# Kernel tuning notes

Measured on AMD Instinct MI355X. Metric: run time of the kernel, lower is better.

The kernel has to match this reference:

```python
import jax, jax.numpy as jnp
import numpy as np

L_IN, L_FREQ, L_OUT = 128, 64, 64
C_IN, C_OUT, T_DIM = 64, 64, 256
SPIN = 1

# ---------- self-contained spin-weighted SHT (MW sampling), replacing s2fft ----------

def _mw_thetas(L, extended):
    n = 2 * L - 1 if extended else L
    return (2 * np.arange(n) + 1) * np.pi / (2 * L - 1)

def _wigner_d_stack(L, thetas, n):
    # d^l_{m,n}(theta) = <l,m| exp(-i theta Jy) |l,n>, computed via eigh of the
    # Hermitian angular-momentum operator Jy. Output (ntheta, L, 2L-1), m at col L-1+m.
    nth = len(thetas)
    out = np.zeros((nth, L, 2 * L - 1), dtype=np.float64)
    for l in range(abs(n), L):
        dim = 2 * l + 1
        m = np.arange(-l, l).astype(np.float64)
        ap = np.sqrt(l * (l + 1.0) - m * (m + 1.0))
        Jy = np.zeros((dim, dim), dtype=np.complex128)
        i = np.arange(dim - 1)
        Jy[i + 1, i] = -0.5j * ap
        Jy[i, i + 1] = 0.5j * ap
        lam, V = np.linalg.eigh(Jy)
        coeff = V * np.conj(V[l + n, :])[None, :]
        phases = np.exp(-1j * np.outer(lam, thetas))
        out[:, l, L - 1 - l:L + l] = (coeff @ phases).T.real
    return out

def _mw_quad_weights(L):
    # per-theta weights on the mirror-extended grid: q_t = (1/(2L-1)) sum_k w(k) e^{ik theta_t}
    # with w(k) = int_0^pi e^{ik t} sin(t) dt
    k = np.arange(-(L - 1), L)
    den = np.where(np.abs(k) == 1, 1, 1 - k * k).astype(np.float64)
    w = np.where(k % 2 == 0, 2.0 / den, 0.0).astype(np.complex128)
    w[k == 1] = 0.5j * np.pi
    w[k == -1] = -0.5j * np.pi
    th = _mw_thetas(L, True)
    return ((w[None, :] * np.exp(1j * np.outer(th, k))).sum(1) / (2 * L - 1)).real

# transform kernels are constants (built once at import, numpy)
_D_FWD = jnp.asarray(_wigner_d_stack(L_IN, _mw_thetas(L_IN, True), -SPIN) * _mw_quad_weights(L_IN)[:, None, None], jnp.float32)
_D_INV = jnp.asarray(_wigner_d_stack(L_OUT, _mw_thetas(L_OUT, False), -SPIN), jnp.float32)
_CL_IN = jnp.asarray(((-1.0) ** SPIN) * np.sqrt((2 * np.arange(L_IN) + 1) / (4 * np.pi)), jnp.float32)
_CL_OUT = jnp.asarray(((-1.0) ** SPIN) * np.sqrt((2 * np.arange(L_OUT) + 1) / (4 * np.pi)), jnp.float32)
_m_all = np.arange(-(L_IN - 1), L_IN)
_PARITY = jnp.asarray(np.where((_m_all + SPIN) % 2 == 0, 1.0, -1.0), jnp.float32)

def sht_forward(x):
    # x: (L_IN, 2*L_IN-1, C) real spatial -> flm: (L_IN, 2*L_IN-1, C) complex, m at L_IN-1+m
    nphi = 2 * L_IN - 1
    ftm = jnp.fft.fftshift(jnp.fft.fft(x, axis=1), axes=1) * (2 * jnp.pi / nphi)
    # mirror extension in theta with (-1)^(m+spin) parity (all channels at once)
    g_ext = jnp.concatenate([ftm, _PARITY[None, :, None] * ftm[::-1][1:]], axis=0)
    flm = jnp.einsum('tlm,tmc->lmc', _D_FWD, g_ext)
    return flm * _CL_IN[:, None, None]

def sht_inverse(flm):
    # flm: (L_OUT, 2*L_OUT-1, C) complex -> (L_OUT, 2*L_OUT-1, C) real spatial
    ftm = jnp.einsum('tlm,lmc->tmc', _D_INV, flm * _CL_OUT[:, None, None])
    return (jnp.fft.ifft(jnp.fft.ifftshift(ftm, axes=1), axis=1) * (2 * L_OUT - 1)).real

def resize_flm(flm, l_in, l_out):
    # centered truncation / zero-pad of (L, 2L-1, C) harmonic coefficients
    if l_out <= l_in:
        d = l_in - l_out
        return flm[:l_out, d:d + 2 * l_out - 1]
    d = l_out - l_in
    return jnp.pad(flm, ((0, d), (d, d), (0, 0)))

# ---------- inputs and parameters ----------

def setup_inputs():
    key = jax.random.key(0)
    ks = jax.random.split(key, 12)
    n = lambda i, shape, s: jax.random.normal(ks[i], shape, jnp.float32) * s
    return {
        'x': jax.random.normal(ks[0], (L_IN, 2 * L_IN - 1, C_IN), jnp.float32),
        't_emb': jax.random.normal(ks[1], (T_DIM,), jnp.float32),
        'spec_conv_w': n(2, (C_IN, C_OUT), (1.0 / C_IN) ** 0.5),
        'spec_conv_b': jnp.zeros((C_OUT,), jnp.float32),
        'spec_wr': n(3, (L_FREQ, C_IN, C_OUT), (0.5 / C_IN) ** 0.5),
        'spec_wi': n(4, (L_FREQ, C_IN, C_OUT), (0.5 / C_IN) ** 0.5),
        'spec_tr_w': n(5, (T_DIM, L_FREQ), (1.0 / T_DIM) ** 0.5),
        'spec_tr_b': jnp.zeros((L_FREQ,), jnp.float32),
        'spec_ti_w': n(6, (T_DIM, L_FREQ), (1.0 / T_DIM) ** 0.5),
        'spec_ti_b': jnp.zeros((L_FREQ,), jnp.float32),
        'spat_conv1_w': n(7, (C_IN, C_OUT), (1.0 / C_IN) ** 0.5),
        'spat_conv1_b': jnp.zeros((C_OUT,), jnp.float32),
        'spat_t_w': n(8, (T_DIM, 2 * C_OUT), (1.0 / T_DIM) ** 0.5),
        'spat_t_b': jnp.zeros((2 * C_OUT,), jnp.float32),
        'spat_weight': n(9, (C_OUT, C_OUT), 0.01),
        'spat_conv2_w': n(10, (C_OUT, C_OUT), (1.0 / C_OUT) ** 0.5),
        'spat_conv2_b': jnp.zeros((C_OUT,), jnp.float32),
        'ln_scale': jnp.ones((C_OUT,), jnp.float32),
        'ln_bias': jnp.zeros((C_OUT,), jnp.float32),
    }

def reference(x, t_emb, spec_conv_w, spec_conv_b, spec_wr, spec_wi, spec_tr_w, spec_tr_b, spec_ti_w, spec_ti_b, spat_conv1_w, spat_conv1_b, spat_t_w, spat_t_b, spat_weight, spat_conv2_w, spat_conv2_b, ln_scale, ln_bias):
    # ----- SphericalSpectralTimeConv branch -----
    flm = sht_forward(x)                                   # (L_IN, 2L_IN-1, C_IN) complex
    flm = resize_flm(flm, L_IN, L_FREQ)                    # (L_FREQ, 2L_FREQ-1, C_IN)
    conv_flm = jnp.einsum('lmi,io->lmo', flm, spec_conv_w) + spec_conv_b
    t_c = (t_emb @ spec_tr_w + spec_tr_b) + 1j * (t_emb @ spec_ti_w + spec_ti_b)   # (L_FREQ,)
    w = t_c[:, None, None] * (spec_wr + 1j * spec_wi)      # (L_FREQ, C_IN, C_OUT)
    flm = jnp.einsum('lmi,lio->lmo', flm, w) + conv_flm
    xs = sht_inverse(resize_flm(flm, L_FREQ, L_OUT))       # (L_OUT, 2L_OUT-1, C_OUT) real
    xs = xs / (jnp.linalg.norm(xs, axis=-1, keepdims=True) + 1e-6)
    # ----- SpatialTimeConv branch (path='down') -----
    h = jnp.einsum('lmi,io->lmo', x, spat_conv1_w) + spat_conv1_b
    t = t_emb @ spat_t_w + spat_t_b
    w_t, b_t = t[:C_OUT], t[C_OUT:]
    h = jnp.einsum('lmi,io->lmo', h, w_t[None, :] * spat_weight)
    h = sht_inverse(resize_flm(sht_forward(h), L_IN, L_OUT))
    h = jnp.einsum('lmi,io->lmo', h, spat_conv2_w) + spat_conv2_b + b_t
    # ----- combine: add, gelu, LayerNorm (eps=1e-6 over channels) -----
    y = jax.nn.gelu(xs + h)
    mu = jnp.mean(y, axis=-1, keepdims=True)
    var = jnp.var(y, axis=-1, keepdims=True)
    return (y - mu) * jax.lax.rsqrt(var + 1e-6) * ln_scale + ln_bias
```

## Files before the change

### kernel.cpp

```cpp
#include <hip/hip_runtime.h>
#include <math.h>

#define DPI 3.141592653589793238462643383279502884

__device__ __forceinline__ float wave_sum64(float v) {
#pragma unroll
  for (int off = 32; off > 0; off >>= 1) v += __shfl_xor(v, off, 64);
  return v;
}

__device__ __forceinline__ float gelu_tanh(float v) {
  float u = 0.7978845608028654f * (v + 0.044715f * v * v * v);
  return 0.5f * v * (1.0f + tanhf(u));
}

#define CN255F ((float)(-2.0 * DPI / 255.0))
#define CN127F ((float)(2.0 * DPI / 127.0))


__device__ __forceinline__ void dft_block(int idx, int tid, const float* __restrict__ x,
                                          float* __restrict__ Are, float* __restrict__ Aim,
                                          float* __restrict__ Bre, float* __restrict__ Bim,
                                          char* sm) {
  float* xs_ = (float*)sm;
  int t = idx >> 2, ph = (idx >> 1) & 1, mh = idx & 1;
  float* ore = ph ? Bre : Are;
  float* oim = ph ? Bim : Aim;
  int pbase = ph * 128;
  int Ktot = ph ? 127 : 128;
  int cg_ = tid & 15, mg = tid >> 4;
  float wr[2], wi[2], rc[2], rs[2];
#pragma unroll
  for (int j = 0; j < 2; ++j) {
    int m = mh * 32 + mg * 2 + j;
    __sincosf(CN255F * (float)m, &rs[j], &rc[j]);
    int r0 = (m * pbase) % 255;
    __sincosf(CN255F * (float)r0, &wi[j], &wr[j]);
  }
  float accr[2][4], acci[2][4];
#pragma unroll
  for (int j = 0; j < 2; ++j)
#pragma unroll
    for (int q = 0; q < 4; ++q) { accr[j][q] = 0.f; acci[j][q] = 0.f; }
  for (int k0 = 0; k0 < Ktot; k0 += 64) {
    int kn = (Ktot - k0 < 64) ? Ktot - k0 : 64;
    __syncthreads();
    {
      const float4* src = (const float4*)(x + ((size_t)t * 255 + pbase + k0) * 64);
      float4* dst = (float4*)xs_;
      int lim = kn * 16;
#pragma unroll
      for (int q = 0; q < 4; ++q) {
        int fidx = tid + q * 256;
        if (fidx < lim) dst[fidx] = src[fidx];
      }
    }
    __syncthreads();
#pragma unroll 2
    for (int k = 0; k < kn; ++k) {
      float4 xv = *(const float4*)&xs_[k * 64 + cg_ * 4];
      float xv4[4] = {xv.x, xv.y, xv.z, xv.w};
#pragma unroll
      for (int j = 0; j < 2; ++j) {
#pragma unroll
        for (int q = 0; q < 4; ++q) {
          accr[j][q] = fmaf(xv4[q], wr[j], accr[j][q]);
          acci[j][q] = fmaf(xv4[q], wi[j], acci[j][q]);
        }
        float nw = wr[j] * rc[j] - wi[j] * rs[j];
        wi[j] = fmaf(wr[j], rs[j], wi[j] * rc[j]);
        wr[j] = nw;
      }
    }
  }
#pragma unroll
  for (int j = 0; j < 2; ++j) {
    int mi = mh * 32 + mg * 2 + j;
    size_t ob = ((size_t)t * 64 + mi) * 64 + cg_ * 4;
    *(float4*)(ore + ob) = make_float4(accr[j][0], accr[j][1], accr[j][2], accr[j][3]);
    *(float4*)(oim + ob) = make_float4(acci[j][0], acci[j][1], acci[j][2], acci[j][3]);
  }
}

__device__ __forceinline__ void wigner_block(int wb, int tid, float* __restrict__ Deff,
                                             float* __restrict__ Dinv, char* sm) {
  float* LF = (float*)sm;
  double* red = (double*)(sm + 512);
  float* clf = (float*)(sm + 1024);
  int mode = (wb < 128) ? 0 : 1;
  int t, mm;
  if (mode == 0) { t = wb; mm = tid; }
  else { mm = wb - 128; t = (tid < 64) ? tid : 63; }
  if (tid < 64) clf[tid] = (float)(-sqrt((2.0 * tid + 1.0) / (4.0 * DPI)));
  if (tid < 128) LF[tid] = (tid == 0) ? 0.f : logf((float)tid);
  __syncthreads();
  for (int s = 1; s < 128; s <<= 1) {
    float add = (tid < 128 && tid >= s) ? LF[tid - s] : 0.f;
    __syncthreads();
    if (tid < 128) LF[tid] += add;
    __syncthreads();
  }
  double denomN = (mode == 0) ? 255.0 : 127.0;
  double beta = (2.0 * t + 1.0) * DPI / denomN;
  float coeff = 1.0f;
  if (mode == 0) {
    if (tid < 63) {
      int k = 2 * (tid + 1);
      red[tid] = 8.0 * cos((double)k * beta) / (1.0 - (double)k * (double)k);
    } else if (tid == 63) {
      red[63] = 4.0;
    }
    __syncthreads();
    for (int s = 32; s > 0; s >>= 1) {
      if (tid < s) red[tid] += red[tid + s];
      __syncthreads();
    }
    double s = red[0] / 255.0;
    if (t == 127) s *= 0.5;
    coeff = (float)(s * (2.0 * DPI / 255.0));
  }
  bool active = (mode == 0) ? (tid < 127) : (tid < 64);
  if (!active) return;
  int m = mm - 63;
  double chd, shd;
  sincos(0.5 * beta, &shd, &chd);
  float cbf = (float)cos(beta);
  float chf = (float)chd, shf = (float)shd;
  int am = (m < 0) ? -m : m;
  int l0v = (am > 1) ? am : 1;
  float seed;
  if (m == 0) {
    seed = -1.4142135623730951f * shf * chf;
  } else {
    int j = am;
    float lch = logf(chf), lsh = logf(shf);
    float e0 = 0.5f * (LF[2 * j] - LF[j - 1] - LF[j + 1]);
    float expo = (m >= 1) ? e0 + (float)(j - 1) * lch + (float)(j + 1) * lsh
                          : e0 + (float)(j + 1) * lch + (float)(j - 1) * lsh;
    float sv = __expf(expo);
    seed = (m >= 1 && ((m + 1) & 1)) ? -sv : sv;
  }
  float dl = seed, dm1 = 0.0f, S_cur = 0.0f;
  float mf = (float)m;
  for (int l = 0; l < 64; ++l) {
    float val = 0.0f;
    if (l >= l0v) {
      val = dl * coeff * clf[l];
      float Ld = (float)l, lp = Ld + 1.0f;
      float S_next = sqrtf((lp * lp - mf * mf) * (lp * lp - 1.0f));
      float num1 = (2.0f * Ld + 1.0f) * (Ld * lp * cbf + mf);
      float dn = (num1 * dl - lp * S_cur * dm1) / (Ld * S_next);
      dm1 = dl; dl = dn; S_cur = S_next;
    }
    if (mode == 0) Deff[((size_t)t * 127 + mm) * 64 + l] = val;
    else Dinv[((size_t)mm * 64 + l) * 64 + t] = val;
  }
}

__device__ __forceinline__ void a2_block(int l, int tid, const float* __restrict__ temb,
                                         const float* __restrict__ trw, const float* __restrict__ trb,
                                         const float* __restrict__ tiw, const float* __restrict__ tib,
                                         const float* __restrict__ scw, const float* __restrict__ swr,
                                         const float* __restrict__ swi, float2* __restrict__ A2,
                                         char* sm) {
  float* fb1 = (float*)sm;
  float* fb2 = (float*)(sm + 1024);
  fb1[tid] = temb[tid] * trw[tid * 64 + l];
  fb2[tid] = temb[tid] * tiw[tid * 64 + l];
  __syncthreads();
  for (int s = 128; s > 0; s >>= 1) {
    if (tid < s) { fb1[tid] += fb1[tid + s]; fb2[tid] += fb2[tid + s]; }
    __syncthreads();
  }
  float tr = fb1[0] + trb[l], ti = fb2[0] + tib[l];
  int o = tid & 63, iq = tid >> 6;
  for (int i = iq * 16; i < iq * 16 + 16; ++i) {
    int idx = (l * 64 + i) * 64 + o;
    float r = swr[idx], s2 = swi[idx];
    A2[idx] = make_float2(scw[i * 64 + o] + tr * r - ti * s2, tr * s2 + ti * r);
  }
}

__device__ __forceinline__ void m_block(int j, int tid, const float* __restrict__ temb,
                                        const float* __restrict__ stw, const float* __restrict__ stb,
                                        const float* __restrict__ c1w, const float* __restrict__ c1b,
                                        const float* __restrict__ sweight, float* __restrict__ Mm,
                                        float* __restrict__ bias2, char* sm) {
  float* fb1 = (float*)sm;
  float* fb2 = (float*)(sm + 1024);
  int o = tid & 63, part = tid >> 6;
  float p = 0.f;
  for (int k = part * 64; k < part * 64 + 64; ++k)
    p = fmaf(temb[k], stw[k * 128 + o], p);
  fb1[part * 64 + o] = p;
  __syncthreads();
  if (part == 0) fb2[o] = fb1[o] + fb1[64 + o] + fb1[128 + o] + fb1[192 + o] + stb[o];
  __syncthreads();
  float tvo = fb2[o];
  float q = 0.f;
  for (int i = part * 16; i < part * 16 + 16; ++i)
    q = fmaf(c1w[j * 64 + i], sweight[i * 64 + o], q);
  __syncthreads();
  fb1[part * 64 + o] = q;
  __syncthreads();
  if (part == 0) Mm[j * 64 + o] = tvo * (fb1[o] + fb1[64 + o] + fb1[128 + o] + fb1[192 + o]);
  if (j == 0) {
    float bq = 0.f;
    for (int i = part * 16; i < part * 16 + 16; ++i)
      bq = fmaf(c1b[i], sweight[i * 64 + o], bq);
    __syncthreads();
    fb1[part * 64 + o] = bq;
    __syncthreads();
    if (part == 0) bias2[o] = tvo * (fb1[o] + fb1[64 + o] + fb1[128 + o] + fb1[192 + o]);
  }
}

__device__ __forceinline__ void tv_block(int tid, const float* __restrict__ temb,
                                         const float* __restrict__ stw, const float* __restrict__ stb,
                                         float* __restrict__ tv, char* sm) {
  float* fb1 = (float*)sm;
  int o = tid & 127, part = tid >> 7;
  float p = 0.f;
  for (int k = part * 128; k < part * 128 + 128; ++k)
    p = fmaf(temb[k], stw[k * 128 + o], p);
  fb1[part * 128 + o] = p;
  __syncthreads();
  if (part == 0) tv[o] = fb1[o] + fb1[128 + o] + stb[o];
}

__global__ __launch_bounds__(256, 2) void ct_pre(
    const float* __restrict__ x, const float* __restrict__ temb,
    const float* __restrict__ trw, const float* __restrict__ trb,
    const float* __restrict__ tiw, const float* __restrict__ tib,
    const float* __restrict__ stw, const float* __restrict__ stb,
    const float* __restrict__ scw, const float* __restrict__ swr,
    const float* __restrict__ swi, const float* __restrict__ c1w,
    const float* __restrict__ c1b, const float* __restrict__ sweight,
    float* __restrict__ Deff, float* __restrict__ Dinv,
    float2* __restrict__ A2, float* __restrict__ Mm,
    float* __restrict__ bias2, float* __restrict__ tv,
    float* __restrict__ ftmA_re, float* __restrict__ ftmA_im,
    float* __restrict__ ftmB_re, float* __restrict__ ftmB_im) {
  __shared__ __align__(16) char sm[16384];
  int vb = blockIdx.x;
  int tid = threadIdx.x;
  if (vb < 255) wigner_block(vb, tid, Deff, Dinv, sm);
  else if (vb < 319) a2_block(vb - 255, tid, temb, trw, trb, tiw, tib, scw, swr, swi, A2, sm);
  else if (vb < 383) m_block(vb - 319, tid, temb, stw, stb, c1w, c1b, sweight, Mm, bias2, sm);
  else if (vb < 384) tv_block(tid, temb, stw, stb, tv, sm);
  else dft_block(vb - 384, tid, x, ftmA_re, ftmA_im, ftmB_re, ftmB_im, sm);
}

__global__ __launch_bounds__(256) void ct_projf(const float* __restrict__ Deff,
                                                const float* __restrict__ fAre,
                                                const float* __restrict__ fAim,
                                                const float* __restrict__ fBre,
                                                const float* __restrict__ fBim,
                                                float* __restrict__ flmA_re, float* __restrict__ flmA_im,
                                                float* __restrict__ flmB_re, float* __restrict__ flmB_im) {
  __shared__ float Dsh[64][32];
  __shared__ float fr_[64][64], fi_[64][64];
  int mm = blockIdx.x, lh = blockIdx.y, th = blockIdx.z;
  float* ore = th ? flmB_re : flmA_re;
  float* oim = th ? flmB_im : flmA_im;
  int tb = th * 64;
  int mi = (mm >= 63) ? (mm - 63) : (63 - mm);
  float csign = (mm >= 63) ? 1.0f : -1.0f;
  int tid = threadIdx.x;
  int cg_ = tid & 15, lg = tid >> 4;
  for (int e = tid; e < 64 * 32; e += 256) {
    int r = e >> 5, li = e & 31;
    Dsh[r][li] = Deff[((size_t)(tb + r) * 127 + mm) * 64 + lh * 32 + li];
  }
  for (int e = tid; e < 64 * 64; e += 256) {
    int r = e >> 6, c = e & 63;
    size_t idx = ((size_t)(tb + r) * 64 + mi) * 64 + c;
    fr_[r][c] = fAre[idx] + fBre[idx];
    fi_[r][c] = csign * (fAim[idx] + fBim[idx]);
  }
  __syncthreads();
  float ar[2][4], ai[2][4];
#pragma unroll
  for (int li = 0; li < 2; ++li)
#pragma unroll
    for (int q = 0; q < 4; ++q) { ar[li][q] = 0.f; ai[li][q] = 0.f; }
#pragma unroll 4
  for (int k = 0; k < 64; ++k) {
    float4 fr4 = *(const float4*)&fr_[k][cg_ * 4];
    float4 fi4 = *(const float4*)&fi_[k][cg_ * 4];
    float2 d2 = *(const float2*)&Dsh[k][lg * 2];
    float frv[4] = {fr4.x, fr4.y, fr4.z, fr4.w};
    float fiv[4] = {fi4.x, fi4.y, fi4.z, fi4.w};
    float dv[2] = {d2.x, d2.y};
#pragma unroll
    for (int li = 0; li < 2; ++li)
#pragma unroll
      for (int q = 0; q < 4; ++q) {
        ar[li][q] = fmaf(dv[li], frv[q], ar[li][q]);
        ai[li][q] = fmaf(dv[li], fiv[q], ai[li][q]);
      }
  }
#pragma unroll
  for (int li = 0; li < 2; ++li) {
    size_t row = ((size_t)mm * 64 + lh * 32 + lg * 2 + li) * 64 + cg_ * 4;
    *(float4*)(ore + row) = make_float4(ar[li][0], ar[li][1], ar[li][2], ar[li][3]);
    *(float4*)(oim + row) = make_float4(ai[li][0], ai[li][1], ai[li][2], ai[li][3]);
  }
}

__global__ __launch_bounds__(256) void ct_mix(const float* __restrict__ flmA_re,
                                              const float* __restrict__ flmA_im,
                                              const float* __restrict__ flmB_re,
                                              const float* __restrict__ flmB_im,
                                              const float2* __restrict__ A2,
                                              const float* __restrict__ Mm,
                                              const float* __restrict__ scb,
                                              const float* __restrict__ bias2,
                                              const float* __restrict__ Deff,
                                              float* __restrict__ s_re, float* __restrict__ s_im,
                                              float* __restrict__ h_re, float* __restrict__ h_im) {
  __shared__ float Ar_[64][32], Ai_[64][32], Msh[64][32];
  __shared__ float Br_[64][65], Bi_[64][65];
  __shared__ float rb[256];
  int l = blockIdx.x, mh = blockIdx.y, oh = blockIdx.z;
  int tid = threadIdx.x;
  int og = tid & 15, mg = tid >> 4;
  rb[tid] = (mh == 0 && tid < 128) ? Deff[((size_t)tid * 127 + 63) * 64 + l] : 0.f;
  __syncthreads();
  for (int s = 128; s > 0; s >>= 1) {
    if (tid < s) rb[tid] += rb[tid + s];
    __syncthreads();
  }
  float slv = rb[0];
  for (int e = tid; e < 64 * 32; e += 256) {
    int r = e >> 5, oi = e & 31;
    float2 aa = A2[((size_t)l * 64 + r) * 64 + oh * 32 + oi];
    Ar_[r][oi] = aa.x; Ai_[r][oi] = aa.y;
    Msh[r][oi] = Mm[r * 64 + oh * 32 + oi];
  }
  for (int e = tid; e < 64 * 64; e += 256) {
    int mi = e >> 6, i = e & 63;
    int gmm = mh * 64 + mi; if (gmm > 126) gmm = 126;
    size_t idx = ((size_t)gmm * 64 + l) * 64 + i;
    Br_[mi][i] = flmA_re[idx] + flmB_re[idx];
    Bi_[mi][i] = flmA_im[idx] + flmB_im[idx];
  }
  __syncthreads();
  int o0 = oh * 32 + og * 2;
  float b0[2] = {scb[o0], scb[o0 + 1]};
  float sr[4][2], si[4][2], hr[4][2], hi[4][2];
#pragma unroll
  for (int jm = 0; jm < 4; ++jm)
#pragma unroll
    for (int qo = 0; qo < 2; ++qo) {
      sr[jm][qo] = b0[qo]; si[jm][qo] = 0.f; hr[jm][qo] = 0.f; hi[jm][qo] = 0.f;
    }
#pragma unroll 4
  for (int k = 0; k < 64; ++k) {
    float2 ar2 = *(const float2*)&Ar_[k][og * 2];
    float2 ai2 = *(const float2*)&Ai_[k][og * 2];
    float2 mv2 = *(const float2*)&Msh[k][og * 2];
    float br4[4], bi4[4];
#pragma unroll
    for (int jm = 0; jm < 4; ++jm) {
      br4[jm] = Br_[mg * 4 + jm][k];
      bi4[jm] = Bi_[mg * 4 + jm][k];
    }
    float arv[2] = {ar2.x, ar2.y}, aiv[2] = {ai2.x, ai2.y}, mvv[2] = {mv2.x, mv2.y};
#pragma unroll
    for (int jm = 0; jm < 4; ++jm)
#pragma unroll
      for (int qo = 0; qo < 2; ++qo) {
        sr[jm][qo] = fmaf(br4[jm], arv[qo], sr[jm][qo]);
        sr[jm][qo] = fmaf(-bi4[jm], aiv[qo], sr[jm][qo]);
        si[jm][qo] = fmaf(br4[jm], aiv[qo], si[jm][qo]);
        si[jm][qo] = fmaf(bi4[jm], arv[qo], si[jm][qo]);
        hr[jm][qo] = fmaf(br4[jm], mvv[qo], hr[jm][qo]);
        hi[jm][qo] = fmaf(bi4[jm], mvv[qo], hi[jm][qo]);
      }
  }
  float bb[2] = {bias2[o0], bias2[o0 + 1]};
#pragma unroll
  for (int jm = 0; jm < 4; ++jm) {
    int gmm = mh * 64 + mg * 4 + jm;
    if (gmm > 126) continue;
    if (gmm == 63) {
#pragma unroll
      for (int qo = 0; qo < 2; ++qo)
        hr[jm][qo] = fmaf(255.0f * slv, bb[qo], hr[jm][qo]);
    }
    size_t row = ((size_t)gmm * 64 + l) * 64 + o0;
    *(float2*)(s_re + row) = make_float2(sr[jm][0], sr[jm][1]);
    *(float2*)(s_im + row) = make_float2(si[jm][0], si[jm][1]);
    *(float2*)(h_re + row) = make_float2(hr[jm][0], hr[jm][1]);
    *(float2*)(h_im + row) = make_float2(hi[jm][0], hi[jm][1]);
  }
}

__global__ __launch_bounds__(256) void ct_proji(const float* __restrict__ Dinv,
                                                const float* __restrict__ s_re,
                                                const float* __restrict__ s_im,
                                                const float* __restrict__ h_re,
                                                const float* __restrict__ h_im,
                                                float* __restrict__ fos_re, float* __restrict__ fos_im,
                                                float* __restrict__ foh_re, float* __restrict__ foh_im) {
  __shared__ float Dsh[64][64];
  __shared__ float Br_[64][32], Bi_[64][32];
  int mm = blockIdx.x, br = blockIdx.y, ch = blockIdx.z;
  const float* ire = br ? h_re : s_re;
  const float* iim = br ? h_im : s_im;
  float* ore = br ? foh_re : fos_re;
  float* oim = br ? foh_im : fos_im;
  int tid = threadIdx.x;
  int cg_ = tid & 15, tg = tid >> 4;
  for (int e = tid; e < 64 * 64; e += 256) {
    int r = e >> 6, tt = e & 63;
    Dsh[r][tt] = Dinv[((size_t)mm * 64 + r) * 64 + tt];
  }
  for (int e = tid; e < 64 * 32; e += 256) {
    int r = e >> 5, cc = e & 31;
    size_t idx = ((size_t)mm * 64 + r) * 64 + ch * 32 + cc;
    Br_[r][cc] = ire[idx];
    Bi_[r][cc] = iim[idx];
  }
  __syncthreads();
  float ar[4][2], ai[4][2];
#pragma unroll
  for (int j = 0; j < 4; ++j)
#pragma unroll
    for (int q = 0; q < 2; ++q) { ar[j][q] = 0.f; ai[j][q] = 0.f; }
#pragma unroll 4
  for (int k = 0; k < 64; ++k) {
    float4 d4 = *(const float4*)&Dsh[k][tg * 4];
    float2 fr2 = *(const float2*)&Br_[k][cg_ * 2];
    float2 fi2 = *(const float2*)&Bi_[k][cg_ * 2];
    float dv[4] = {d4.x, d4.y, d4.z, d4.w};
    float frv[2] = {fr2.x, fr2.y}, fiv[2] = {fi2.x, fi2.y};
#pragma unroll
    for (int j = 0; j < 4; ++j)
#pragma unroll
      for (int q = 0; q < 2; ++q) {
        ar[j][q] = fmaf(dv[j], frv[q], ar[j][q]);
        ai[j][q] = fmaf(dv[j], fiv[q], ai[j][q]);
      }
  }
#pragma unroll
  for (int j = 0; j < 4; ++j) {
    int t = tg * 4 + j;
    size_t ob = ((size_t)t * 127 + mm) * 64 + ch * 32 + cg_ * 2;
    *(float2*)(ore + ob) = make_float2(ar[j][0], ar[j][1]);
    *(float2*)(oim + ob) = make_float2(ai[j][0], ai[j][1]);
  }
}

__global__ __launch_bounds__(256) void ct_idft(const float* __restrict__ fos_re,
                                               const float* __restrict__ fos_im,
                                               const float* __restrict__ foh_re,
                                               const float* __restrict__ foh_im,
                                               float* __restrict__ xsbA, float* __restrict__ xsbB,
                                               float* __restrict__ hsbA, float* __restrict__ hsbB) {
  __shared__ float Br_[32][64], Bi_[32][64];
  int t = blockIdx.x, br = blockIdx.y;
  int z = blockIdx.z;
  int ph = z >> 1, kh = z & 1;
  const float* fre = br ? foh_re : fos_re;
  const float* fim = br ? foh_im : fos_im;
  float* outp = br ? (kh ? hsbB : hsbA) : (kh ? xsbB : xsbA);
  int kbase = kh * 64;
  int Ktot = kh ? 63 : 64;
  int tid = threadIdx.x;
  int cg_ = tid & 15, pg = tid >> 4;
  float wc[4], ws[4], rc[4], rs[4];
#pragma unroll
  for (int j = 0; j < 4; ++j) {
    int gp = ph * 64 + pg * 4 + j; if (gp > 126) gp = 126;
    __sincosf(CN127F * (float)gp, &rs[j], &rc[j]);
    int r0 = ((kbase - 63) * gp) % 127;
    __sincosf(CN127F * (float)r0, &ws[j], &wc[j]);
  }
  float acc[4][4];
#pragma unroll
  for (int j = 0; j < 4; ++j)
#pragma unroll
    for (int q = 0; q < 4; ++q) acc[j][q] = 0.f;
  for (int k0 = 0; k0 < Ktot; k0 += 32) {
    int kn = (Ktot - k0 < 32) ? Ktot - k0 : 32;
    __syncthreads();
    for (int e = tid; e < 32 * 64; e += 256) {
      int r = e >> 6, j = e & 63;
      if (r < kn) {
        size_t bidx = ((size_t)t * 127 + kbase + k0 + r) * 64 + j;
        Br_[r][j] = fre[bidx]; Bi_[r][j] = fim[bidx];
      }
    }
    __syncthreads();
#pragma unroll 2
    for (int k = 0; k < kn; ++k) {
      float4 b_r = *(const float4*)&Br_[k][cg_ * 4];
      float4 b_i = *(const float4*)&Bi_[k][cg_ * 4];
      float brv[4] = {b_r.x, b_r.y, b_r.z, b_r.w};
      float biv[4] = {b_i.x, b_i.y, b_i.z, b_i.w};
#pragma unroll
      for (int j = 0; j < 4; ++j) {
#pragma unroll
        for (int q = 0; q < 4; ++q) {
          acc[j][q] = fmaf(brv[q], wc[j], acc[j][q]);
          acc[j][q] = fmaf(biv[q], -ws[j], acc[j][q]);
        }
        float nw = wc[j] * rc[j] - ws[j] * rs[j];
        ws[j] = fmaf(wc[j], rs[j], ws[j] * rc[j]);
        wc[j] = nw;
      }
    }
  }
#pragma unroll
  for (int j = 0; j < 4; ++j) {
    int gp = ph * 64 + pg * 4 + j;
    if (gp > 126) continue;
    *(float4*)(outp + ((size_t)t * 127 + gp) * 64 + cg_ * 4) =
        make_float4(acc[j][0], acc[j][1], acc[j][2], acc[j][3]);
  }
}

__global__ __launch_bounds__(256) void ct_fin(const float* __restrict__ xsbA,
                                              const float* __restrict__ xsbB,
                                              const float* __restrict__ hsbA,
                                              const float* __restrict__ hsbB,
                                              const float* __restrict__ c2w,
                                              const float* __restrict__ c2b,
                                              const float* __restrict__ tv,
                                              const float* __restrict__ lns,
                                              const float* __restrict__ lnb,
                                              float* __restrict__ out) {
  int w = threadIdx.x >> 6, lane = threadIdx.x & 63;
  size_t row = (size_t)blockIdx.x * 4 + w;
  size_t base = row * 64 + lane;
  float hv = hsbA[base] + hsbB[base];
  float xv = xsbA[base] + xsbB[base];
  float acc = c2b[lane] + tv[64 + lane];
#pragma unroll 16
  for (int i = 0; i < 64; ++i)
    acc = fmaf(__shfl(hv, i, 64), c2w[i * 64 + lane], acc);
  float ss = wave_sum64(xv * xv);
  xv = xv / (sqrtf(ss) + 1e-6f);
  float y = xv + acc;
  float g = gelu_tanh(y);
  float mu = wave_sum64(g) * (1.0f / 64.0f);
  float d = g - mu;
  float var = wave_sum64(d * d) * (1.0f / 64.0f);
  out[base] = d * rsqrtf(var + 1e-6f) * lns[lane] + lnb[lane];
}

extern "C" void kernel_launch(void* const* d_in, const int* in_sizes, int n_in,
                              void* d_out, int out_size, void* d_ws, size_t ws_size,
                              hipStream_t stream) {
  const float* x = (const float*)d_in[0];
  const float* temb = (const float*)d_in[1];
  const float* scw = (const float*)d_in[2];
  const float* scb = (const float*)d_in[3];
  const float* swr = (const float*)d_in[4];
  const float* swi = (const float*)d_in[5];
  const float* strw = (const float*)d_in[6];
  const float* strb = (const float*)d_in[7];
  const float* stiw = (const float*)d_in[8];
  const float* stib = (const float*)d_in[9];
  const float* c1w = (const float*)d_in[10];
  const float* c1b = (const float*)d_in[11];
  const float* stw = (const float*)d_in[12];
  const float* stb = (const float*)d_in[13];
  const float* sweight = (const float*)d_in[14];
  const float* c2w = (const float*)d_in[15];
  const float* c2b = (const float*)d_in[16];
  const float* lns = (const float*)d_in[17];
  const float* lnb = (const float*)d_in[18];
  float* out = (float*)d_out;

  char* base = (char*)d_ws;
  size_t off = 0;
  auto alloc = [&](size_t bytes) -> void* {
    void* p = base + off;
    off += (bytes + 255) & ~(size_t)255;
    return p;
  };
  float* tv = (float*)alloc(128 * sizeof(float));
  float* Mm = (float*)alloc(4096 * sizeof(float));
  float* bias2 = (float*)alloc(64 * sizeof(float));
  float2* A2 = (float2*)alloc(262144 * sizeof(float2));
  float* Deff = (float*)alloc(1040384 * sizeof(float));
  float* Dinv = (float*)alloc(520192 * sizeof(float));
  float* ftmA_re = (float*)alloc(524288 * sizeof(float));
  float* ftmA_im = (float*)alloc(524288 * sizeof(float));
  float* ftmB_re = (float*)alloc(524288 * sizeof(float));
  float* ftmB_im = (float*)alloc(524288 * sizeof(float));
  float* flmA_re = (float*)alloc(520192 * sizeof(float));
  float* flmA_im = (float*)alloc(520192 * sizeof(float));
  float* flmB_re = (float*)alloc(520192 * sizeof(float));
  float* flmB_im = (float*)alloc(520192 * sizeof(float));
  if (off > ws_size) return;
  float* s_re = ftmA_re;
  float* s_im = ftmA_im;
  float* h_re = ftmB_re;
  float* h_im = ftmB_im;
  float* fos_re = Deff;
  float* fos_im = Deff + 520192;
  float* foh_re = flmA_re;
  float* foh_im = flmA_im;
  float* xsbA = flmB_re;
  float* xsbB = flmB_im;
  float* hsbA = ftmA_re;
  float* hsbB = ftmA_im;

  hipLaunchKernelGGL(ct_pre, dim3(896), dim3(256), 0, stream,
                     x, temb, strw, strb, stiw, stib, stw, stb,
                     scw, swr, swi, c1w, c1b, sweight,
                     Deff, Dinv, A2, Mm, bias2, tv,
                     ftmA_re, ftmA_im, ftmB_re, ftmB_im);
  hipLaunchKernelGGL(ct_projf, dim3(127, 2, 2), dim3(256), 0, stream, Deff,
                     ftmA_re, ftmA_im, ftmB_re, ftmB_im,
                     flmA_re, flmA_im, flmB_re, flmB_im);
  hipLaunchKernelGGL(ct_mix, dim3(64, 2, 2), dim3(256), 0, stream,
                     flmA_re, flmA_im, flmB_re, flmB_im, A2, Mm, scb, bias2, Deff,
                     s_re, s_im, h_re, h_im);
  hipLaunchKernelGGL(ct_proji, dim3(127, 2, 2), dim3(256), 0, stream, Dinv,
                     s_re, s_im, h_re, h_im, fos_re, fos_im, foh_re, foh_im);
  hipLaunchKernelGGL(ct_idft, dim3(64, 2, 4), dim3(256), 0, stream,
                     fos_re, fos_im, foh_re, foh_im, xsbA, xsbB, hsbA, hsbB);
  hipLaunchKernelGGL(ct_fin, dim3(2032), dim3(256), 0, stream, xsbA, xsbB, hsbA, hsbB,
                     c2w, c2b, tv, lns, lnb, out);
}
```

Baseline: 193.9 us.

## Fuse six kernel launches into one persistent kernel with grid barriers

Merges the six pipeline stages (pre, forward projection, mixing, inverse projection, inverse DFT, final layernorm) into one persistent kernel. Blocks loop over per-stage tile indices and meet at atomic-counter grid barriers that are reset by a memset before launch. This removes inter-kernel launch gaps and tail drain. The cost is one large shared-memory allocation, which caps occupancy, plus spin-wait barriers that assume all blocks are co-resident. The Wigner recurrence also switches to fast reciprocal and sqrt intrinsics.

```diff
diff --git a/kernel.cpp b/kernel.cpp
--- a/kernel.cpp
+++ b/kernel.cpp
@@ -2,6 +2,8 @@
 #include <math.h>
 
 #define DPI 3.141592653589793238462643383279502884
+#define CN255F ((float)(-2.0 * DPI / 255.0))
+#define CN127F ((float)(2.0 * DPI / 127.0))
 
 __device__ __forceinline__ float wave_sum64(float v) {
 #pragma unroll
@@ -14,11 +16,21 @@
   return 0.5f * v * (1.0f + tanhf(u));
 }
 
-#define CN255F ((float)(-2.0 * DPI / 255.0))
-#define CN127F ((float)(2.0 * DPI / 127.0))
-
-
-__device__ __forceinline__ void dft_block(int idx, int tid, const float* __restrict__ x,
+__device__ __forceinline__ void gsync(unsigned* cnt, unsigned nb) {
+  __syncthreads();
+  if (threadIdx.x == 0) {
+    __threadfence();
+    atomicAdd(cnt, 1u);
+    while (__hip_atomic_load(cnt, __ATOMIC_RELAXED, __HIP_MEMORY_SCOPE_AGENT) < nb) {
+      __builtin_amdgcn_s_sleep(2);
+    }
+    __threadfence();
+  }
+  __syncthreads();
+}
+
+
+__device__ __forceinline__ void dft_phase(int idx, int tid, const float* __restrict__ x,
                                           float* __restrict__ Are, float* __restrict__ Aim,
                                           float* __restrict__ Bre, float* __restrict__ Bim,
                                           char* sm) {
@@ -82,7 +94,7 @@
   }
 }
 
-__device__ __forceinline__ void wigner_block(int wb, int tid, float* __restrict__ Deff,
+__device__ __forceinline__ void wigner_phase(int wb, int tid, float* __restrict__ Deff,
                                              float* __restrict__ Dinv, char* sm) {
   float* LF = (float*)sm;
   double* red = (double*)(sm + 512);
@@ -120,44 +132,45 @@
     coeff = (float)(s * (2.0 * DPI / 255.0));
   }
   bool active = (mode == 0) ? (tid < 127) : (tid < 64);
-  if (!active) return;
-  int m = mm - 63;
-  double chd, shd;
-  sincos(0.5 * beta, &shd, &chd);
-  float cbf = (float)cos(beta);
-  float chf = (float)chd, shf = (float)shd;
-  int am = (m < 0) ? -m : m;
-  int l0v = (am > 1) ? am : 1;
-  float seed;
-  if (m == 0) {
-    seed = -1.4142135623730951f * shf * chf;
-  } else {
-    int j = am;
-    float lch = logf(chf), lsh = logf(shf);
-    float e0 = 0.5f * (LF[2 * j] - LF[j - 1] - LF[j + 1]);
-    float expo = (m >= 1) ? e0 + (float)(j - 1) * lch + (float)(j + 1) * lsh
-                          : e0 + (float)(j + 1) * lch + (float)(j - 1) * lsh;
-    float sv = __expf(expo);
-    seed = (m >= 1 && ((m + 1) & 1)) ? -sv : sv;
-  }
-  float dl = seed, dm1 = 0.0f, S_cur = 0.0f;
-  float mf = (float)m;
-  for (int l = 0; l < 64; ++l) {
-    float val = 0.0f;
-    if (l >= l0v) {
-      val = dl * coeff * clf[l];
-      float Ld = (float)l, lp = Ld + 1.0f;
-      float S_next = sqrtf((lp * lp - mf * mf) * (lp * lp - 1.0f));
-      float num1 = (2.0f * Ld + 1.0f) * (Ld * lp * cbf + mf);
-      float dn = (num1 * dl - lp * S_cur * dm1) / (Ld * S_next);
-      dm1 = dl; dl = dn; S_cur = S_next;
-    }
-    if (mode == 0) Deff[((size_t)t * 127 + mm) * 64 + l] = val;
-    else Dinv[((size_t)mm * 64 + l) * 64 + t] = val;
-  }
-}
-
-__device__ __forceinline__ void a2_block(int l, int tid, const float* __restrict__ temb,
+  if (active) {
+    int m = mm - 63;
+    double chd, shd;
+    sincos(0.5 * beta, &shd, &chd);
+    float cbf = (float)cos(beta);
+    float chf = (float)chd, shf = (float)shd;
+    int am = (m < 0) ? -m : m;
+    int l0v = (am > 1) ? am : 1;
+    float seed;
+    if (m == 0) {
+      seed = -1.4142135623730951f * shf * chf;
+    } else {
+      int j = am;
+      float lch = logf(chf), lsh = logf(shf);
+      float e0 = 0.5f * (LF[2 * j] - LF[j - 1] - LF[j + 1]);
+      float expo = (m >= 1) ? e0 + (float)(j - 1) * lch + (float)(j + 1) * lsh
+                            : e0 + (float)(j + 1) * lch + (float)(j - 1) * lsh;
+      float sv = __expf(expo);
+      seed = (m >= 1 && ((m + 1) & 1)) ? -sv : sv;
+    }
+    float dl = seed, dm1 = 0.0f, S_cur = 0.0f;
+    float mf = (float)m;
+    for (int l = 0; l < 64; ++l) {
+      float val = 0.0f;
+      if (l >= l0v) {
+        val = dl * coeff * clf[l];
+        float Ld = (float)l, lp = Ld + 1.0f;
+        float S_next = __fsqrt_rn((lp * lp - mf * mf) * (lp * lp - 1.0f));
+        float num1 = (2.0f * Ld + 1.0f) * (Ld * lp * cbf + mf);
+        float dn = (num1 * dl - lp * S_cur * dm1) * __fdividef(1.0f, Ld * S_next);
+        dm1 = dl; dl = dn; S_cur = S_next;
+      }
+      if (mode == 0) Deff[((size_t)t * 127 + mm) * 64 + l] = val;
+      else Dinv[((size_t)mm * 64 + l) * 64 + t] = val;
+    }
+  }
+}
+
+__device__ __forceinline__ void a2_phase(int l, int tid, const float* __restrict__ temb,
                                          const float* __restrict__ trw, const float* __restrict__ trb,
                                          const float* __restrict__ tiw, const float* __restrict__ tib,
                                          const float* __restrict__ scw, const float* __restrict__ swr,
@@ -181,7 +194,7 @@
   }
 }
 
-__device__ __forceinline__ void m_block(int j, int tid, const float* __restrict__ temb,
+__device__ __forceinline__ void m_phase(int j, int tid, const float* __restrict__ temb,
                                         const float* __restrict__ stw, const float* __restrict__ stb,
                                         const float* __restrict__ c1w, const float* __restrict__ c1b,
                                         const float* __restrict__ sweight, float* __restrict__ Mm,
@@ -215,7 +228,7 @@
   }
 }
 
-__device__ __forceinline__ void tv_block(int tid, const float* __restrict__ temb,
+__device__ __forceinline__ void tv_phase(int tid, const float* __restrict__ temb,
                                          const float* __restrict__ stw, const float* __restrict__ stb,
                                          float* __restrict__ tv, char* sm) {
   float* fb1 = (float*)sm;
@@ -228,45 +241,21 @@
   if (part == 0) tv[o] = fb1[o] + fb1[128 + o] + stb[o];
 }
 
-__global__ __launch_bounds__(256, 2) void ct_pre(
-    const float* __restrict__ x, const float* __restrict__ temb,
-    const float* __restrict__ trw, const float* __restrict__ trb,
-    const float* __restrict__ tiw, const float* __restrict__ tib,
-    const float* __restrict__ stw, const float* __restrict__ stb,
-    const float* __restrict__ scw, const float* __restrict__ swr,
-    const float* __restrict__ swi, const float* __restrict__ c1w,
-    const float* __restrict__ c1b, const float* __restrict__ sweight,
-    float* __restrict__ Deff, float* __restrict__ Dinv,
-    float2* __restrict__ A2, float* __restrict__ Mm,
-    float* __restrict__ bias2, float* __restrict__ tv,
-    float* __restrict__ ftmA_re, float* __restrict__ ftmA_im,
-    float* __restrict__ ftmB_re, float* __restrict__ ftmB_im) {
-  __shared__ __align__(16) char sm[16384];
-  int vb = blockIdx.x;
-  int tid = threadIdx.x;
-  if (vb < 255) wigner_block(vb, tid, Deff, Dinv, sm);
-  else if (vb < 319) a2_block(vb - 255, tid, temb, trw, trb, tiw, tib, scw, swr, swi, A2, sm);
-  else if (vb < 383) m_block(vb - 319, tid, temb, stw, stb, c1w, c1b, sweight, Mm, bias2, sm);
-  else if (vb < 384) tv_block(tid, temb, stw, stb, tv, sm);
-  else dft_block(vb - 384, tid, x, ftmA_re, ftmA_im, ftmB_re, ftmB_im, sm);
-}
-
-__global__ __launch_bounds__(256) void ct_projf(const float* __restrict__ Deff,
-                                                const float* __restrict__ fAre,
-                                                const float* __restrict__ fAim,
-                                                const float* __restrict__ fBre,
-                                                const float* __restrict__ fBim,
-                                                float* __restrict__ flmA_re, float* __restrict__ flmA_im,
-                                                float* __restrict__ flmB_re, float* __restrict__ flmB_im) {
-  __shared__ float Dsh[64][32];
-  __shared__ float fr_[64][64], fi_[64][64];
-  int mm = blockIdx.x, lh = blockIdx.y, th = blockIdx.z;
+__device__ __forceinline__ void projf_phase(int mm, int lh, int th, int tid,
+                                            const float* __restrict__ Deff,
+                                            const float* __restrict__ fAre, const float* __restrict__ fAim,
+                                            const float* __restrict__ fBre, const float* __restrict__ fBim,
+                                            float* __restrict__ flmA_re, float* __restrict__ flmA_im,
+                                            float* __restrict__ flmB_re, float* __restrict__ flmB_im,
+                                            char* sm) {
+  float (*Dsh)[32] = (float(*)[32])(sm);
+  float (*fr_)[64] = (float(*)[64])(sm + 8192);
+  float (*fi_)[64] = (float(*)[64])(sm + 24576);
   float* ore = th ? flmB_re : flmA_re;
   float* oim = th ? flmB_im : flmA_im;
   int tb = th * 64;
   int mi = (mm >= 63) ? (mm - 63) : (63 - mm);
   float csign = (mm >= 63) ? 1.0f : -1.0f;
-  int tid = threadIdx.x;
   int cg_ = tid & 15, lg = tid >> 4;
   for (int e = tid; e < 64 * 32; e += 256) {
     int r = e >> 5, li = e & 31;
@@ -308,22 +297,21 @@
   }
 }
 
-__global__ __launch_bounds__(256) void ct_mix(const float* __restrict__ flmA_re,
-                                              const float* __restrict__ flmA_im,
-                                              const float* __restrict__ flmB_re,
-                                              const float* __restrict__ flmB_im,
-                                              const float2* __restrict__ A2,
-                                              const float* __restrict__ Mm,
-                                              const float* __restrict__ scb,
-                                              const float* __restrict__ bias2,
-                                              const float* __restrict__ Deff,
-                                              float* __restrict__ s_re, float* __restrict__ s_im,
-                                              float* __restrict__ h_re, float* __restrict__ h_im) {
-  __shared__ float Ar_[64][32], Ai_[64][32], Msh[64][32];
-  __shared__ float Br_[64][65], Bi_[64][65];
-  __shared__ float rb[256];
-  int l = blockIdx.x, mh = blockIdx.y, oh = blockIdx.z;
-  int tid = threadIdx.x;
+__device__ __forceinline__ void mix_phase(int l, int mh, int oh, int tid,
+                                          const float* __restrict__ flmA_re, const float* __restrict__ flmA_im,
+                                          const float* __restrict__ flmB_re, const float* __restrict__ flmB_im,
+                                          const float2* __restrict__ A2, const float* __restrict__ Mm,
+                                          const float* __restrict__ scb, const float* __restrict__ bias2,
+                                          const float* __restrict__ Deff,
+                                          float* __restrict__ s_re, float* __restrict__ s_im,
+                                          float* __restrict__ h_re, float* __restrict__ h_im,
+                                          char* sm) {
+  float (*Ar_)[32] = (float(*)[32])(sm);
+  float (*Ai_)[32] = (float(*)[32])(sm + 8192);
+  float (*Msh)[32] = (float(*)[32])(sm + 16384);
+  float (*Br_)[65] = (float(*)[65])(sm + 24576);
+  float (*Bi_)[65] = (float(*)[65])(sm + 41216);
+  float* rb = (float*)(sm + 57856);
   int og = tid & 15, mg = tid >> 4;
   rb[tid] = (mh == 0 && tid < 128) ? Deff[((size_t)tid * 127 + 63) * 64 + l] : 0.f;
   __syncthreads();
@@ -397,21 +385,20 @@
   }
 }
 
-__global__ __launch_bounds__(256) void ct_proji(const float* __restrict__ Dinv,
-                                                const float* __restrict__ s_re,
-                                                const float* __restrict__ s_im,
-                                                const float* __restrict__ h_re,
-                                                const float* __restrict__ h_im,
-                                                float* __restrict__ fos_re, float* __restrict__ fos_im,
-                                                float* __restrict__ foh_re, float* __restrict__ foh_im) {
-  __shared__ float Dsh[64][64];
-  __shared__ float Br_[64][32], Bi_[64][32];
-  int mm = blockIdx.x, br = blockIdx.y, ch = blockIdx.z;
+__device__ __forceinline__ void proji_phase(int mm, int br, int ch, int tid,
+                                            const float* __restrict__ Dinv,
+                                            const float* __restrict__ s_re, const float* __restrict__ s_im,
+                                            const float* __restrict__ h_re, const float* __restrict__ h_im,
+                                            float* __restrict__ fos_re, float* __restrict__ fos_im,
+                                            float* __restrict__ foh_re, float* __restrict__ foh_im,
+                                            char* sm) {
+  float (*Dsh)[64] = (float(*)[64])(sm);
+  float (*Br_)[32] = (float(*)[32])(sm + 16384);
+  float (*Bi_)[32] = (float(*)[32])(sm + 24576);
   const float* ire = br ? h_re : s_re;
   const float* iim = br ? h_im : s_im;
   float* ore = br ? foh_re : fos_re;
   float* oim = br ? foh_im : fos_im;
-  int tid = threadIdx.x;
   int cg_ = tid & 15, tg = tid >> 4;
   for (int e = tid; e < 64 * 64; e += 256) {
     int r = e >> 6, tt = e & 63;
@@ -453,22 +440,13 @@
   }
 }
 
-__global__ __launch_bounds__(256) void ct_idft(const float* __restrict__ fos_re,
-                                               const float* __restrict__ fos_im,
-                                               const float* __restrict__ foh_re,
-                                               const float* __restrict__ foh_im,
-                                               float* __restrict__ xsbA, float* __restrict__ xsbB,
-                                               float* __restrict__ hsbA, float* __restrict__ hsbB) {
-  __shared__ float Br_[32][64], Bi_[32][64];
-  int t = blockIdx.x, br = blockIdx.y;
-  int z = blockIdx.z;
-  int ph = z >> 1, kh = z & 1;
-  const float* fre = br ? foh_re : fos_re;
-  const float* fim = br ? foh_im : fos_im;
-  float* outp = br ? (kh ? hsbB : hsbA) : (kh ? xsbB : xsbA);
+__device__ __forceinline__ void idft_phase(int t, int ph, int kh, int tid,
+                                           const float* __restrict__ fre, const float* __restrict__ fim,
+                                           float* __restrict__ outp, char* sm) {
+  float (*Br_)[64] = (float(*)[64])(sm);
+  float (*Bi_)[64] = (float(*)[64])(sm + 8192);
   int kbase = kh * 64;
   int Ktot = kh ? 63 : 64;
-  int tid = threadIdx.x;
   int cg_ = tid & 15, pg = tid >> 4;
   float wc[4], ws[4], rc[4], rs[4];
 #pragma unroll
@@ -522,33 +500,119 @@
   }
 }
 
-__global__ __launch_bounds__(256) void ct_fin(const float* __restrict__ xsbA,
-                                              const float* __restrict__ xsbB,
-                                              const float* __restrict__ hsbA,
-                                              const float* __restrict__ hsbB,
-                                              const float* __restrict__ c2w,
-                                              const float* __restrict__ c2b,
-                                              const float* __restrict__ tv,
-                                              const float* __restrict__ lns,
-                                              const float* __restrict__ lnb,
-                                              float* __restrict__ out) {
-  int w = threadIdx.x >> 6, lane = threadIdx.x & 63;
-  size_t row = (size_t)blockIdx.x * 4 + w;
-  size_t base = row * 64 + lane;
-  float hv = hsbA[base] + hsbB[base];
-  float xv = xsbA[base] + xsbB[base];
-  float acc = c2b[lane] + tv[64 + lane];
+__global__ __launch_bounds__(256, 2) void ct_all(
+    const float* __restrict__ x, const float* __restrict__ temb,
+    const float* __restrict__ trw, const float* __restrict__ trb,
+    const float* __restrict__ tiw, const float* __restrict__ tib,
+    const float* __restrict__ stw, const float* __restrict__ stb,
+    const float* __restrict__ scw, const float* __restrict__ swr,
+    const float* __restrict__ swi, const float* __restrict__ c1w,
+    const float* __restrict__ c1b, const float* __restrict__ sweight,
+    const float* __restrict__ c2w, const float* __restrict__ c2b,
+    const float* __restrict__ lns, const float* __restrict__ lnb,
+    char* __restrict__ ws, float* __restrict__ out,
+    const float* __restrict__ scb) {
+  __shared__ __align__(16) char sm[58880];
+  int bid = blockIdx.x;
+  int tid = threadIdx.x;
+  unsigned G = gridDim.x;
+
+  float* tv = (float*)(ws + 0);
+  float* Mm = (float*)(ws + 512);
+  float* bias2 = (float*)(ws + 16896);
+  float2* A2 = (float2*)(ws + 17152);
+  float* Deff = (float*)(ws + 2114304);
+  float* Dinv = (float*)(ws + 6275840);
+  float* ftmA_re = (float*)(ws + 8356608);
+  float* ftmA_im = (float*)(ws + 10453760);
+  float* ftmB_re = (float*)(ws + 12550912);
+  float* ftmB_im = (float*)(ws + 14648064);
+  float* flmA_re = (float*)(ws + 16745216);
+  float* flmA_im = (float*)(ws + 18825984);
+  float* flmB_re = (float*)(ws + 20906752);
+  float* flmB_im = (float*)(ws + 22987520);
+  unsigned* cnt = (unsigned*)(ws + 25068288);
+  float* s_re = ftmA_re;
+  float* s_im = ftmA_im;
+  float* h_re = ftmB_re;
+  float* h_im = ftmB_im;
+  float* fos_re = Deff;
+  float* fos_im = Deff + 520192;
+  float* foh_re = flmA_re;
+  float* foh_im = flmA_im;
+  float* xsbA = flmB_re;
+  float* xsbB = flmB_im;
+  float* hsbA = ftmA_re;
+  float* hsbB = ftmA_im;
+
+  for (int tile = bid; tile < 896; tile += G) {
+    __syncthreads();
+    if (tile < 512) {
+      dft_phase(tile, tid, x, ftmA_re, ftmA_im, ftmB_re, ftmB_im, sm);
+    } else {
+      int sb = tile - 512;
+      if (sb < 255) wigner_phase(sb, tid, Deff, Dinv, sm);
+      else if (sb < 319) a2_phase(sb - 255, tid, temb, trw, trb, tiw, tib, scw, swr, swi, A2, sm);
+      else if (sb < 383) m_phase(sb - 319, tid, temb, stw, stb, c1w, c1b, sweight, Mm, bias2, sm);
+      else tv_phase(tid, temb, stw, stb, tv, sm);
+    }
+  }
+  gsync(cnt + 0, G);
+
+  for (int tile = bid; tile < 508; tile += G) {
+    __syncthreads();
+    projf_phase(tile >> 2, (tile >> 1) & 1, tile & 1, tid, Deff,
+                ftmA_re, ftmA_im, ftmB_re, ftmB_im,
+                flmA_re, flmA_im, flmB_re, flmB_im, sm);
+  }
+  gsync(cnt + 1, G);
+
+  for (int tile = bid; tile < 256; tile += G) {
+    __syncthreads();
+    mix_phase(tile >> 2, (tile >> 1) & 1, tile & 1, tid,
+              flmA_re, flmA_im, flmB_re, flmB_im, A2, Mm, scb, bias2, Deff,
+              s_re, s_im, h_re, h_im, sm);
+  }
+  gsync(cnt + 2, G);
+
+  for (int tile = bid; tile < 508; tile += G) {
+    __syncthreads();
+    proji_phase(tile >> 2, (tile >> 1) & 1, tile & 1, tid, Dinv,
+                s_re, s_im, h_re, h_im, fos_re, fos_im, foh_re, foh_im, sm);
+  }
+  gsync(cnt + 3, G);
+
+  for (int tile = bid; tile < 512; tile += G) {
+    __syncthreads();
+    int t = tile >> 3, br = (tile >> 2) & 1, z = tile & 3;
+    int ph = z >> 1, kh = z & 1;
+    const float* fre = br ? foh_re : fos_re;
+    const float* fim = br ? foh_im : fos_im;
+    float* outp = br ? (kh ? hsbB : hsbA) : (kh ? xsbB : xsbA);
+    idft_phase(t, ph, kh, tid, fre, fim, outp, sm);
+  }
+  gsync(cnt + 4, G);
+
+  {
+    int w = tid >> 6, lane = tid & 63;
+    for (int row = bid * 4 + w; row < 8128; row += G * 4) {
+      size_t base = (size_t)row * 64 + lane;
+      float hv = hsbA[base] + hsbB[base];
+      float xv = xsbA[base] + xsbB[base];
+      float acc = c2b[lane] + tv[64 + lane];
 #pragma unroll 16
-  for (int i = 0; i < 64; ++i)
-    acc = fmaf(__shfl(hv, i, 64), c2w[i * 64 + lane], acc);
-  float ss = wave_sum64(xv * xv);
-  xv = xv / (sqrtf(ss) + 1e-6f);
-  float y = xv + acc;
-  float g = gelu_tanh(y);
-  float mu = wave_sum64(g) * (1.0f / 64.0f);
-  float d = g - mu;
-  float var = wave_sum64(d * d) * (1.0f / 64.0f);
-  out[base] = d * rsqrtf(var + 1e-6f) * lns[lane] + lnb[lane];
+      for (int i = 0; i < 64; ++i)
+        acc = fmaf(__shfl(hv, i, 64), c2w[i * 64 + lane], acc);
+      float ss = wave_sum64(xv * xv);
+      xv = xv / (sqrtf(ss) + 1e-6f);
+      float y = xv + acc;
+      float g = gelu_tanh(y);
+      float mu = wave_sum64(g) * (1.0f / 64.0f);
+      float d = g - mu;
+      float var = wave_sum64(d * d) * (1.0f / 64.0f);
+      out[base] = d * rsqrtf(var + 1e-6f) * lns[lane] + lnb[lane];
+    }
+  }
 }
 
 extern "C" void kernel_launch(void* const* d_in, const int* in_sizes, int n_in,
@@ -574,57 +638,27 @@
   const float* lns = (const float*)d_in[17];
   const float* lnb = (const float*)d_in[18];
   float* out = (float*)d_out;
-
-  char* base = (char*)d_ws;
-  size_t off = 0;
-  auto alloc = [&](size_t bytes) -> void* {
-    void* p = base + off;
-    off += (bytes + 255) & ~(size_t)255;
-    return p;
-  };
-  float* tv = (float*)alloc(128 * sizeof(float));
-  float* Mm = (float*)alloc(4096 * sizeof(float));
-  float* bias2 = (float*)alloc(64 * sizeof(float));
-  float2* A2 = (float2*)alloc(262144 * sizeof(float2));
-  float* Deff = (float*)alloc(1040384 * sizeof(float));
-  float* Dinv = (float*)alloc(520192 * sizeof(float));
-  float* ftmA_re = (float*)alloc(524288 * sizeof(float));
-  float* ftmA_im = (float*)alloc(524288 * sizeof(float));
-  float* ftmB_re = (float*)alloc(524288 * sizeof(float));
-  float* ftmB_im = (float*)alloc(524288 * sizeof(float));
-  float* flmA_re = (float*)alloc(520192 * sizeof(float));
-  float* flmA_im = (float*)alloc(520192 * sizeof(float));
-  float* flmB_re = (float*)alloc(520192 * sizeof(float));
-  float* flmB_im = (float*)alloc(520192 * sizeof(float));
-  if (off > ws_size) return;
-  float* s_re = ftmA_re;
-  float* s_im = ftmA_im;
-  float* h_re = ftmB_re;
-  float* h_im = ftmB_im;
-  float* fos_re = Deff;
-  float* fos_im = Deff + 520192;
-  float* foh_re = flmA_re;
-  float* foh_im = flmA_im;
-  float* xsbA = flmB_re;
-  float* xsbB = flmB_im;
-  float* hsbA = ftmA_re;
-  float* hsbB = ftmA_im;
-
-  hipLaunchKernelGGL(ct_pre, dim3(896), dim3(256), 0, stream,
+  char* wsb = (char*)d_ws;
+
+  if (ws_size < 25068288 + 256) return;
+
+  static int g_grid = 0;
+  if (g_grid == 0) {
+    int perCU = 0;
+    (void)hipOccupancyMaxActiveBlocksPerMultiprocessor(&perCU, (const void*)ct_all, 256, 0);
+    int dev = 0, nCU = 0;
+    (void)hipGetDevice(&dev);
+    (void)hipDeviceGetAttribute(&nCU, hipDeviceAttributeMultiprocessorCount, dev);
+    int g = perCU * nCU;
+    if (g <= 0) g = 448;
+    if (g > 512) g = 512;
+    g_grid = g;
+  }
+
+  hipMemsetAsync(wsb + 25068288, 0, 256, stream);
+
+  hipLaunchKernelGGL(ct_all, dim3(g_grid), dim3(256), 0, stream,
                      x, temb, strw, strb, stiw, stib, stw, stb,
-                     scw, swr, swi, c1w, c1b, sweight,
-                     Deff, Dinv, A2, Mm, bias2, tv,
-                     ftmA_re, ftmA_im, ftmB_re, ftmB_im);
-  hipLaunchKernelGGL(ct_projf, dim3(127, 2, 2), dim3(256), 0, stream, Deff,
-                     ftmA_re, ftmA_im, ftmB_re, ftmB_im,
-                     flmA_re, flmA_im, flmB_re, flmB_im);
-  hipLaunchKernelGGL(ct_mix, dim3(64, 2, 2), dim3(256), 0, stream,
-                     flmA_re, flmA_im, flmB_re, flmB_im, A2, Mm, scb, bias2, Deff,
-                     s_re, s_im, h_re, h_im);
-  hipLaunchKernelGGL(ct_proji, dim3(127, 2, 2), dim3(256), 0, stream, Dinv,
-                     s_re, s_im, h_re, h_im, fos_re, fos_im, foh_re, foh_im);
-  hipLaunchKernelGGL(ct_idft, dim3(64, 2, 4), dim3(256), 0, stream,
-                     fos_re, fos_im, foh_re, foh_im, xsbA, xsbB, hsbA, hsbB);
-  hipLaunchKernelGGL(ct_fin, dim3(2032), dim3(256), 0, stream, xsbA, xsbB, hsbA, hsbB,
-                     c2w, c2b, tv, lns, lnb, out);
-}
+                     scw, swr, swi, c1w, c1b, sweight, c2w, c2b, lns, lnb,
+                     wsb, out, scb);
+}
```

Measured after the change: 352.2 us. +81.6%, slower.
